# Performance work log

Measured on AMD Instinct MI355X. Metric: run time of the kernel, lower is better.

## Reference

```python
import jax, jax.numpy as jnp
import numpy as np
import math

D_MODEL = 128
N_HEADS = 8
D_K = D_MODEL // N_HEADS
D_FF = 512
N_LAYERS = 3
N_BUCKETS = 32
EPS = 1e-5
NEG_INF = -1e9
SCALE = 1.0 / math.sqrt(D_K)


def _hier_adj_np(N, L=8):
    # deterministic hierarchical edges from ExpanderGraphBuilder.build_hierarchical_edges
    stride = max(1, int(math.sqrt(N / L)))
    layer_size = N // L if L <= N else 1
    A = np.zeros((N, N), dtype=np.float32)
    for l in range(min(L, N)):
        start = l * layer_size
        end = min(start + layer_size, N)
        for i in range(start, end):
            A[i, max(start, i - stride):min(end, i + stride + 1)] = 1.0
            A[i, i] = 0.0
    return np.maximum(A, A.T)


def _build_mask(h, depot_idx=0):
    # h: (B,N,D). Returns additive mask (B,N+1,N+1) incl. global node.
    B, N, _ = h.shape
    k = min(max(1, math.ceil(math.log2(N))), N - 1)
    sq = jnp.sum(h * h, axis=-1)
    d2 = sq[:, :, None] + sq[:, None, :] - 2.0 * jnp.einsum('bnd,bmd->bnm', h, h)
    d2 = d2 + jnp.where(jnp.eye(N, dtype=bool), jnp.inf, 0.0)
    _, knn_idx = jax.lax.top_k(-d2, k)  # (B,N,k) nearest neighbors
    b_ix = jnp.arange(B)[:, None, None]
    i_ix = jnp.arange(N)[None, :, None]
    adj = jnp.zeros((B, N, N), dtype=h.dtype).at[b_ix, i_ix, knn_idx].set(1.0)
    adj = jnp.maximum(adj, adj.transpose(0, 2, 1))  # symmetrize knn
    adj = jnp.maximum(adj, jnp.asarray(_hier_adj_np(N))[None])
    adj = adj.at[:, depot_idx, :].set(1.0)
    adj = adj.at[:, :, depot_idx].set(1.0)
    adj = jnp.maximum(adj, jnp.eye(N, dtype=h.dtype)[None])
    full = jnp.ones((B, N + 1, N + 1), dtype=h.dtype).at[:, :N, :N].set(adj)
    return jnp.where(full > 0, 0.0, NEG_INF).astype(h.dtype)


def _inorm(x, w, b):
    # InstanceNorm1d over node dim per channel (x: (B,N1,D))
    mu = jnp.mean(x, axis=1, keepdims=True)
    var = jnp.mean(jnp.square(x - mu), axis=1, keepdims=True)
    return (x - mu) * jax.lax.rsqrt(var + EPS) * w + b


def _ega_layer(hg, bucket, mask, Wq, Wk, Wv, Wo, emb, W1, b1, W2, b2, n1w, n1b, n2w, n2b):
    B, N1, D = hg.shape
    heads = lambda x: x.reshape(B, N1, N_HEADS, D_K).transpose(0, 2, 1, 3)
    Q, K, V = heads(hg @ Wq.T), heads(hg @ Wk.T), heads(hg @ Wv.T)
    scores = jnp.einsum('bhnd,bhmd->bhnm', Q, K) * SCALE
    # rel_scores[b,h,i,j] = <Q[b,h,i], emb[bucket[b,i,j], h]> : contract with the
    # 32-entry table first, then gather - same math, no (B,H,N,N,Dk) intermediate.
    qe = jnp.einsum('bhnd,khd->bhnk', Q, emb.reshape(N_BUCKETS, N_HEADS, D_K))
    rel = jnp.take_along_axis(qe, jnp.broadcast_to(bucket[:, None], (B, N_HEADS, N1, N1)), axis=3)
    attn = jax.nn.softmax(scores + rel + mask[:, None], axis=-1)
    ctx = jnp.einsum('bhnm,bhmd->bhnd', attn, V).transpose(0, 2, 1, 3).reshape(B, N1, D)
    h1 = _inorm(hg + ctx @ Wo.T, n1w, n1b)
    ffn = jax.nn.relu(h1 @ W1.T + b1) @ W2.T + b2
    return _inorm(h1 + ffn, n2w, n2b)


def _forward(coords, in_W, in_b, gnode, Wq, Wk, Wv, Wo, emb, W1, b1, W2, b2,
             n1_w, n1_b, n2_w, n2_b, out_W, out_b):
    B, N, _ = coords.shape
    h = coords @ in_W.T + in_b
    g = jnp.broadcast_to(gnode, (B, 1, D_MODEL)).astype(h.dtype)
    # distance buckets over coords extended with the global node at (0,0)
    coords_ext = jnp.concatenate([coords, jnp.zeros((B, 1, 2), coords.dtype)], axis=1)
    diff = coords_ext[:, :, None, :] - coords_ext[:, None, :, :]
    dist = jax.lax.stop_gradient(jnp.sqrt(jnp.sum(diff * diff, axis=-1)))
    bucket = jnp.clip((dist * N_BUCKETS).astype(jnp.int32), 0, N_BUCKETS - 1)  # (B,N+1,N+1)
    pools = []
    for l in range(N_LAYERS):
        g = g + h.mean(axis=1, keepdims=True)
        hg = jnp.concatenate([h, g], axis=1)
        mask = _build_mask(jax.lax.stop_gradient(h))  # torch builds adj via .item(): detached
        hg = _ega_layer(hg, bucket, mask, Wq[l], Wk[l], Wv[l], Wo[l], emb[l],
                        W1[l], b1[l], W2[l], b2[l], n1_w[l], n1_b[l], n2_w[l], n2_b[l])
        h, g = hg[:, :N], hg[:, N:]
        pools.append(h.mean(axis=1))
    p_multi = jnp.stack(pools, axis=1).mean(axis=1)
    E_static = (h + p_multi[:, None, :]) @ out_W.T + out_b
    return E_static, p_multi


def setup_inputs():
    key = jax.random.key(0)
    ks = jax.random.split(key, 24)
    B, N, L = 2, 1024, N_LAYERS
    def nrm(k, shape, s=0.05):
        return jax.random.normal(k, shape, dtype=jnp.float32) * s
    return {
        'coords': jax.random.uniform(ks[0], (B, N, 2), dtype=jnp.float32),
        'in_W': nrm(ks[1], (D_MODEL, 2), 0.5),
        'in_b': nrm(ks[2], (D_MODEL,)),
        'gnode': nrm(ks[3], (1, 1, D_MODEL), 0.2),
        'Wq': nrm(ks[4], (L, D_MODEL, D_MODEL)),
        'Wk': nrm(ks[5], (L, D_MODEL, D_MODEL)),
        'Wv': nrm(ks[6], (L, D_MODEL, D_MODEL)),
        'Wo': nrm(ks[7], (L, D_MODEL, D_MODEL)),
        'emb': nrm(ks[8], (L, N_BUCKETS, N_HEADS * D_K)),
        'W1': nrm(ks[9], (L, D_FF, D_MODEL)),
        'b1': nrm(ks[10], (L, D_FF)),
        'W2': nrm(ks[11], (L, D_MODEL, D_FF)),
        'b2': nrm(ks[12], (L, D_MODEL)),
        'n1_w': jnp.ones((L, D_MODEL), jnp.float32) + nrm(ks[13], (L, D_MODEL)),
        'n1_b': nrm(ks[14], (L, D_MODEL)),
        'n2_w': jnp.ones((L, D_MODEL), jnp.float32) + nrm(ks[15], (L, D_MODEL)),
        'n2_b': nrm(ks[16], (L, D_MODEL)),
        'out_W': nrm(ks[17], (D_MODEL, D_MODEL)),
        'out_b': nrm(ks[18], (D_MODEL,)),
    }


def reference(coords, in_W, in_b, gnode, Wq, Wk, Wv, Wo, emb, W1, b1, W2, b2,
              n1_w, n1_b, n2_w, n2_b, out_W, out_b):
    return _forward(coords, in_W, in_b, gnode, Wq, Wk, Wv, Wo, emb, W1, b1, W2, b2,
                    n1_w, n1_b, n2_w, n2_b, out_W, out_b)
```

## Files before the change

kernel.cpp:

```cpp
#include <hip/hip_runtime.h>

#define BB 2
#define NN 1024
#define N1 1025
#define DM 128
#define NH 8
#define DK 16
#define DFF 512
#define NBUK 32
#define NLAYERS 3
#define KNN_K 10
#define ADJW 17
#define BSTR 1088
#define NSPLIT 8
#define BIGF 3.0e38f
#define SM_OFF 24.0f

#define PWQ_OFF 0
#define PWK_OFF 49152
#define PWV_OFF 98304
#define PWO_OFF 147456
#define PW1_OFF 196608
#define PW2_OFF 393216
#define PWOUT_OFF 589824
#define PWQE_OFF 606208
#define PW_TOT 704512

#define PBLK 344
#define NBNODE 1024
#define EBLK (NBNODE + BB)
#define BBLK 8713

#define KSEL_BLK 512
#define QKV_GX 33
#define QKV_BLK (QKV_GX * 40)
#define OSUM_N (BB * NH * N1 * 16)
#define ZTOT (OSUM_N + BB * NH * N1)

typedef __attribute__((ext_vector_type(8))) short bf8;
typedef __attribute__((ext_vector_type(4))) float f4;
typedef unsigned short u16;
typedef unsigned int u32;

__device__ __forceinline__ u16 f2bf(float x) {
  unsigned u = __float_as_uint(x);
  return (u16)((u + 0x7fff + ((u >> 16) & 1)) >> 16);
}
__device__ __forceinline__ float bf2f(u16 u) {
  return __uint_as_float(((unsigned)u) << 16);
}
__device__ __forceinline__ bf8 mk8(ushort4 a, ushort4 b) {
  bf8 r;
  r[0] = (short)a.x; r[1] = (short)a.y; r[2] = (short)a.z; r[3] = (short)a.w;
  r[4] = (short)b.x; r[5] = (short)b.y; r[6] = (short)b.z; r[7] = (short)b.w;
  return r;
}

__global__ __launch_bounds__(256) void init_kernel(
    const float* __restrict__ coords, const float* __restrict__ inW,
    const float* __restrict__ inb, const float* __restrict__ gnode,
    const float* __restrict__ Wq, const float* __restrict__ Wk,
    const float* __restrict__ Wv, const float* __restrict__ Wo,
    const float* __restrict__ W1, const float* __restrict__ W2,
    const float* __restrict__ oW, const float* __restrict__ emb,
    u16* __restrict__ PH, u16* __restrict__ PL,
    float* __restrict__ X, u16* __restrict__ XH, u16* __restrict__ XM,
    u16* __restrict__ XL, unsigned char* __restrict__ buckp) {
  int blk = blockIdx.x;
  if (blk < PBLK) {
    int idx = blk * 256 + threadIdx.x;
    if (idx >= 88064) return;
    if (idx >= 75776) {
      int rel = idx - 75776;
      int lane = rel & 63, g = rel >> 6;
      int ks = g & 3, nt = g >> 2;
      int n = nt * 16 + (lane & 15);
      int k = ks * 32 + (lane >> 4) * 8;
      int l = n >> 8; int c = n & 255; int h = c >> 5, bk = c & 31;
      const float* e = emb + ((size_t)l * NBUK + bk) * DM + h * DK;
      const float* wq = Wq + ((size_t)l * DM + h * DK) * DM;
      u16* ph = PH + (size_t)idx * 8;
      u16* pl = PL + (size_t)idx * 8;
      #pragma unroll
      for (int q = 0; q < 8; ++q) {
        float s = 0.f;
        #pragma unroll
        for (int d = 0; d < DK; ++d) s += e[d] * wq[(size_t)d * DM + k + q];
        u16 hh = f2bf(s);
        ph[q] = hh;
        pl[q] = f2bf(s - bf2f(hh));
      }
      return;
    }
    const float* W; int rel, Kdim;
    if (idx < 24576) {
      int seg = idx / 6144; rel = idx % 6144; Kdim = 128;
      W = seg == 0 ? Wq : seg == 1 ? Wk : seg == 2 ? Wv : Wo;
    } else if (idx < 49152) { rel = idx - 24576; Kdim = 128; W = W1; }
    else if (idx < 73728)   { rel = idx - 49152; Kdim = 512; W = W2; }
    else                    { rel = idx - 73728; Kdim = 128; W = oW; }
    int lane = rel & 63;
    int g = rel >> 6;
    int ksteps = Kdim >> 5;
    int ks = g % ksteps, nt = g / ksteps;
    int n = nt * 16 + (lane & 15);
    int k = ks * 32 + (lane >> 4) * 8;
    const float* p = W + (size_t)n * Kdim + k;
    u16* ph = PH + (size_t)idx * 8;
    u16* pl = PL + (size_t)idx * 8;
    #pragma unroll
    for (int q = 0; q < 8; ++q) {
      float x = p[q];
      u16 hh = f2bf(x);
      ph[q] = hh;
      pl[q] = f2bf(x - bf2f(hh));
    }
    return;
  }
  if (blk < PBLK + EBLK) {
    int eb = blk - PBLK;
    if (eb >= NBNODE) {
      int b = eb - NBNODE;
      int t = threadIdx.x;
      if (t >= 128) return;
      int lane = t & 63;
      float sx = 0.f, sy = 0.f;
      for (int n = lane; n < NN; n += 64) {
        float2 c = *(const float2*)(coords + (size_t)(b * NN + n) * 2);
        sx += c.x; sy += c.y;
      }
      #pragma unroll
      for (int o = 1; o < 64; o <<= 1) { sx += __shfl_xor(sx, o); sy += __shfl_xor(sy, o); }
      float mx = sx * (1.0f / NN), my = sy * (1.0f / NN);
      int d = t;
      size_t id = ((size_t)b * N1 + NN) * DM + d;
      float v = gnode[d] + inb[d] + mx * inW[d * 2 + 0] + my * inW[d * 2 + 1];
      X[id] = v;
      u16 hh = f2bf(v); float r1 = v - bf2f(hh);
      u16 mm = f2bf(r1);
      XH[id] = hh; XM[id] = mm; XL[id] = f2bf(r1 - bf2f(mm));
      return;
    }
    int idx = eb * 256 + threadIdx.x;
    if (idx >= BB * NN * DM) return;
    int d = idx % DM; int r = idx / DM; int n = r % NN; int b = r / NN;
    float cx = coords[(b * NN + n) * 2 + 0], cy = coords[(b * NN + n) * 2 + 1];
    size_t id = ((size_t)b * N1 + n) * DM + d;
    float v = cx * inW[d * 2 + 0] + cy * inW[d * 2 + 1] + inb[d];
    X[id] = v;
    u16 hh = f2bf(v); float r1 = v - bf2f(hh);
    u16 mm = f2bf(r1);
    XH[id] = hh; XM[id] = mm; XL[id] = f2bf(r1 - bf2f(mm));
    return;
  }
  int idx = (blk - PBLK - EBLK) * 256 + threadIdx.x;
  if (idx >= BB * N1 * BSTR) return;
  int j = idx % BSTR; int r = idx / BSTR; int i = r % N1; int b = r / N1;
  unsigned char v = 0;
  if (j < N1) {
    float xi = 0.f, yi = 0.f, xj = 0.f, yj = 0.f;
    if (i < NN) { xi = coords[(b * NN + i) * 2]; yi = coords[(b * NN + i) * 2 + 1]; }
    if (j < NN) { xj = coords[(b * NN + j) * 2]; yj = coords[(b * NN + j) * 2 + 1]; }
    float dx = xi - xj, dy = yi - yj;
    float dist = sqrtf(dx * dx + dy * dy);
    int bu = (int)(dist * 32.0f);
    bu = bu < 0 ? 0 : (bu > 31 ? 31 : bu);
    v = (unsigned char)bu;
  }
  buckp[idx] = v;
}

__global__ __launch_bounds__(256) void gram_kernel(
    const u16* __restrict__ XH, const u16* __restrict__ XM, const u16* __restrict__ XL,
    unsigned long long* __restrict__ adj, float* __restrict__ d2) {
  __shared__ __align__(16) u16 AsH[32][72];
  __shared__ __align__(16) u16 AsM[32][72];
  __shared__ __align__(16) u16 AsL[32][72];
  __shared__ __align__(16) u16 BsH[64][72];
  __shared__ __align__(16) u16 BsM[64][72];
  __shared__ __align__(16) u16 BsL[64][72];
  __shared__ float sqS[64];
  int b = blockIdx.z;
  int m0 = blockIdx.x * 32, n0 = blockIdx.y * 64;
  size_t boff = (size_t)b * N1;
  int t = threadIdx.x;

  {
    int flat = blockIdx.x + 32 * (blockIdx.y + 16 * blockIdx.z);
    int tid = flat * 256 + t;
    if (tid < BB * N1 * ADJW) adj[tid] = 0ull;
  }

  int lane = t & 63, w = t >> 6;
  int wm = (w >> 1) * 16, wn = (w & 1) * 32;
  int quad = lane >> 4, r16 = lane & 15;

  f4 acc0 = {0.f, 0.f, 0.f, 0.f}, acc1 = {0.f, 0.f, 0.f, 0.f};
  int ar = t >> 3, as_ = (t & 7) * 8;
  int br = t >> 2, bs_ = (t & 3) * 16;
  int sqrow = t >> 2, sqk = (t & 3) * 16;
  float mySq = 0.f;

  for (int k0 = 0; k0 < DM; k0 += 64) {
    {
      size_t src = (boff + m0 + ar) * DM + k0 + as_;
      *(bf8*)&AsH[ar][as_] = *(const bf8*)(XH + src);
      *(bf8*)&AsM[ar][as_] = *(const bf8*)(XM + src);
      *(bf8*)&AsL[ar][as_] = *(const bf8*)(XL + src);
    }
    {
      size_t src = (boff + n0 + br) * DM + k0 + bs_;
      *(bf8*)&BsH[br][bs_] = *(const bf8*)(XH + src);
      *(bf8*)&BsH[br][bs_ + 8] = *(const bf8*)(XH + src + 8);
      *(bf8*)&BsM[br][bs_] = *(const bf8*)(XM + src);
      *(bf8*)&BsM[br][bs_ + 8] = *(const bf8*)(XM + src + 8);
      *(bf8*)&BsL[br][bs_] = *(const bf8*)(XL + src);
      *(bf8*)&BsL[br][bs_ + 8] = *(const bf8*)(XL + src + 8);
    }
    __syncthreads();
    #pragma unroll
    for (int ks = 0; ks < 64; ks += 16) {
      int seg = (quad & 1) * 8;
      bf8 aHM = *(const bf8*)((quad < 2) ? &AsH[wm + r16][ks + seg] : &AsM[wm + r16][ks + seg]);
      bf8 aHL = *(const bf8*)((quad < 2) ? &AsH[wm + r16][ks + seg] : &AsL[wm + r16][ks + seg]);
      #pragma unroll
      for (int tt = 0; tt < 2; ++tt) {
        int nr = wn + tt * 16 + r16;
        bf8 bH = *(const bf8*)&BsH[nr][ks + seg];
        bf8 bM = *(const bf8*)&BsM[nr][ks + seg];
        bf8 b3 = *(const bf8*)((quad < 2) ? &BsL[nr][ks + seg] : &BsH[nr][ks + seg]);
        f4& a = tt ? acc1 : acc0;
        a = __builtin_amdgcn_mfma_f32_16x16x32_bf16(aHM, bH, a, 0, 0, 0);
        a = __builtin_amdgcn_mfma_f32_16x16x32_bf16(aHM, bM, a, 0, 0, 0);
        a = __builtin_amdgcn_mfma_f32_16x16x32_bf16(aHL, b3, a, 0, 0, 0);
      }
    }
    #pragma unroll
    for (int half = 0; half < 2; ++half) {
      bf8 hv = *(const bf8*)&BsH[sqrow][sqk + half * 8];
      bf8 mv = *(const bf8*)&BsM[sqrow][sqk + half * 8];
      bf8 lv = *(const bf8*)&BsL[sqrow][sqk + half * 8];
      #pragma unroll
      for (int q = 0; q < 8; ++q) {
        float x = (bf2f((u16)hv[q]) + bf2f((u16)mv[q])) + bf2f((u16)lv[q]);
        mySq += x * x;
      }
    }
    __syncthreads();
  }
  mySq += __shfl_xor(mySq, 1);
  mySq += __shfl_xor(mySq, 2);
  if ((t & 3) == 0) sqS[sqrow] = mySq;
  __syncthreads();

  #pragma unroll
  for (int tt = 0; tt < 2; ++tt) {
    f4 a = tt ? acc1 : acc0;
    int nl = wn + tt * 16 + r16;
    int n = n0 + nl;
    float sj = sqS[nl];
    #pragma unroll
    for (int reg = 0; reg < 4; ++reg) {
      int m = m0 + wm + quad * 4 + reg;
      float v = (m == n) ? BIGF : (sj - 2.f * a[reg]);
      d2[((size_t)b * NN + m) * NN + n] = v;
    }
  }
}

__global__ __launch_bounds__(256) void knnqkv_kernel(
    const float* __restrict__ d2, unsigned long long* __restrict__ adj,
    const u16* __restrict__ AH, const u16* __restrict__ AL,
    const u16* __restrict__ Pbase_H, const u16* __restrict__ Pbase_L,
    size_t offQ, size_t offK, size_t offV, size_t offE,
    u16* __restrict__ QH, u16* __restrict__ QL,
    u16* __restrict__ KH, u16* __restrict__ KL, u16* __restrict__ Vbf,
    float* __restrict__ qe_all, float* __restrict__ zbuf, int M) {
  __shared__ float dd[4][NN];
  {
    int ztid = blockIdx.x * 256 + threadIdx.x;
    if (ztid < ZTOT) zbuf[ztid] = 0.f;
  }
  int blk = blockIdx.x;
  if (blk < KSEL_BLK) {
    int b = blk / (NN / 4);
    int i0 = (blk % (NN / 4)) * 4;
    int t = threadIdx.x, lane = t & 63, w = t >> 6;

    const float4* src = (const float4*)(d2 + ((size_t)b * NN + i0) * NN);
    float4* dst = (float4*)&dd[0][0];
    #pragma unroll
    for (int x = 0; x < 4; ++x) dst[t + x * 256] = src[t + x * 256];
    __syncthreads();

    int i = i0 + w;
    for (int it = 0; it < KNN_K; ++it) {
      float bv = BIGF; int bi = 0x3fffffff;
      for (int j = lane; j < NN; j += 64) {
        float v = dd[w][j];
        if (v < bv) { bv = v; bi = j; }
      }
      #pragma unroll
      for (int o = 1; o < 64; o <<= 1) {
        float ov = __shfl_xor(bv, o); int oi = __shfl_xor(bi, o);
        if (ov < bv || (ov == bv && oi < bi)) { bv = ov; bi = oi; }
      }
      if (lane == 0) {
        dd[w][bi] = BIGF;
        atomicOr(&adj[((size_t)b * N1 + i) * ADJW + (bi >> 6)], 1ull << (bi & 63));
        atomicOr(&adj[((size_t)b * N1 + bi) * ADJW + (i >> 6)], 1ull << (i & 63));
      }
    }
    return;
  }
  int rel = blk - KSEL_BLK;
  int gx = rel % QKV_GX;
  int y = rel / QKV_GX;
  int z, nt;
  if (y < 8) { z = 0; nt = y; }
  else if (y < 16) { z = 1; nt = y - 8; }
  else if (y < 24) { z = 2; nt = y - 16; }
  else { z = 3; nt = y - 24; }
  size_t woff = z == 0 ? offQ : (z == 1 ? offK : (z == 2 ? offV : offE));
  const u16* PH = Pbase_H + woff;
  const u16* PL = Pbase_L + woff;
  int lane = threadIdx.x & 63;
  int quad = lane >> 4, r16 = lane & 15;
  int mt = gx * 4 + (threadIdx.x >> 6);
  f4 acc = {0.f, 0.f, 0.f, 0.f};
  int m0 = mt * 16;
  int mrow = m0 + r16; if (mrow >= M) mrow = M - 1;
  const u16* aph = AH + (size_t)mrow * DM + quad * 8;
  const u16* apl = AL + (size_t)mrow * DM + quad * 8;
  const u16* ph = PH + ((size_t)nt * 4 * 64 + lane) * 8;
  const u16* pl = PL + ((size_t)nt * 4 * 64 + lane) * 8;
  #pragma unroll
  for (int ks = 0; ks < 4; ++ks) {
    bf8 aH = *(const bf8*)(aph);
    bf8 aL = *(const bf8*)(apl);
    aph += 32; apl += 32;
    bf8 bH = *(const bf8*)(ph + (size_t)ks * 512);
    bf8 bL = *(const bf8*)(pl + (size_t)ks * 512);
    acc = __builtin_amdgcn_mfma_f32_16x16x32_bf16(aH, bH, acc, 0, 0, 0);
    acc = __builtin_amdgcn_mfma_f32_16x16x32_bf16(aH, bL, acc, 0, 0, 0);
    acc = __builtin_amdgcn_mfma_f32_16x16x32_bf16(aL, bH, acc, 0, 0, 0);
  }
  if (m0 >= M) return;
  int n = nt * 16 + r16;
  #pragma unroll
  for (int reg = 0; reg < 4; ++reg) {
    int m = m0 + quad * 4 + reg;
    if (m >= M) continue;
    float v = acc[reg];
    if (z == 3) {
      int b = m / N1, nr = m % N1;
      int h = n >> 5, bk = n & 31;
      qe_all[(((size_t)b * NH + h) * N1 + nr) * 32 + bk] = v;
      continue;
    }
    size_t oi = (size_t)m * DM + n;
    if (z == 0) {
      float sv = v * 0.25f;
      u16 hh = f2bf(sv);
      QH[oi] = hh;
      QL[oi] = f2bf(sv - bf2f(hh));
    } else if (z == 1) {
      u16 hh = f2bf(v);
      KH[oi] = hh;
      KL[oi] = f2bf(v - bf2f(hh));
    } else {
      Vbf[oi] = f2bf(v);
    }
  }
}

__device__ __forceinline__ void gemm_dev16(
    const u16* __restrict__ AH, const u16* __restrict__ AL,
    const u16* __restrict__ PH, const u16* __restrict__ PL,
    const float* __restrict__ bias, const float* __restrict__ res,
    float* __restrict__ outF, u16* __restrict__ outH, u16* __restrict__ outL,
    int M, int Kdim, int Nout, int relu, int mt, int nt) {
  int lane = threadIdx.x & 63;
  int quad = lane >> 4, r16 = lane & 15;
  int ksteps = Kdim >> 5;
  f4 acc = {0.f, 0.f, 0.f, 0.f};

  int m0 = mt * 16;
  int mrow = m0 + r16; if (mrow >= M) mrow = M - 1;
  const u16* aph = AH + (size_t)mrow * Kdim + quad * 8;
  const u16* apl = AL + (size_t)mrow * Kdim + quad * 8;
  const u16* ph = PH + ((size_t)nt * ksteps * 64 + lane) * 8;
  const u16* pl = PL + ((size_t)nt * ksteps * 64 + lane) * 8;

  #pragma unroll 4
  for (int ks = 0; ks < ksteps; ++ks) {
    bf8 aH = *(const bf8*)(aph);
    bf8 aL = *(const bf8*)(apl);
    aph += 32; apl += 32;
    bf8 bH = *(const bf8*)(ph + (size_t)ks * 512);
    bf8 bL = *(const bf8*)(pl + (size_t)ks * 512);
    acc = __builtin_amdgcn_mfma_f32_16x16x32_bf16(aH, bH, acc, 0, 0, 0);
    acc = __builtin_amdgcn_mfma_f32_16x16x32_bf16(aH, bL, acc, 0, 0, 0);
    acc = __builtin_amdgcn_mfma_f32_16x16x32_bf16(aL, bH, acc, 0, 0, 0);
  }

  if (m0 >= M) return;
  int n = nt * 16 + r16;
  #pragma unroll
  for (int reg = 0; reg < 4; ++reg) {
    int m = m0 + quad * 4 + reg;
    if (m < M) {
      float v = acc[reg];
      if (bias) v += bias[n];
      if (relu) v = fmaxf(v, 0.f);
      if (res) v += res[(size_t)m * Nout + n];
      size_t oi = (size_t)m * Nout + n;
      if (outF) outF[oi] = v;
      if (outH) {
        u16 hh = f2bf(v);
        outH[oi] = hh;
        outL[oi] = f2bf(v - bf2f(hh));
      }
    }
  }
}

__global__ __launch_bounds__(256) void gemm_kernel(
    const u16* __restrict__ AH, const u16* __restrict__ AL,
    const u16* __restrict__ PH, const u16* __restrict__ PL,
    const float* __restrict__ bias, const float* __restrict__ res,
    float* __restrict__ outF, u16* __restrict__ outH, u16* __restrict__ outL,
    int M, int Kdim, int Nout, int relu) {
  gemm_dev16(AH, AL, PH, PL, bias, res, outF, outH, outL, M, Kdim, Nout, relu,
             blockIdx.x * 4 + (threadIdx.x >> 6), blockIdx.y);
}

__global__ __launch_bounds__(256) void gemm_wo_kernel(
    const float* __restrict__ Osum, const float* __restrict__ lsum,
    const u16* __restrict__ PH, const u16* __restrict__ PL,
    const float* __restrict__ res, float* __restrict__ outF, int M) {
  int lane = threadIdx.x & 63;
  int quad = lane >> 4, r16 = lane & 15;
  int mt = blockIdx.x * 4 + (threadIdx.x >> 6), nt = blockIdx.y;
  f4 acc = {0.f, 0.f, 0.f, 0.f};
  int m0 = mt * 16;
  int mrow = m0 + r16; if (mrow >= M) mrow = M - 1;
  int b = mrow / N1, nr = mrow % N1;
  const u16* ph = PH + ((size_t)nt * 4 * 64 + lane) * 8;
  const u16* pl = PL + ((size_t)nt * 4 * 64 + lane) * 8;
  #pragma unroll
  for (int ks = 0; ks < 4; ++ks) {
    int k = ks * 32 + quad * 8;
    int h = k >> 4, d0 = k & 15;
    size_t base = (size_t)(b * NH + h) * N1 + nr;
    float inv = 1.0f / lsum[base];
    const float* op = Osum + base * 16 + d0;
    bf8 aH, aL;
    #pragma unroll
    for (int j = 0; j < 8; ++j) {
      float v = op[j] * inv;
      u16 hh = f2bf(v);
      aH[j] = (short)hh;
      aL[j] = (short)f2bf(v - bf2f(hh));
    }
    bf8 bH = *(const bf8*)(ph + (size_t)ks * 512);
    bf8 bL = *(const bf8*)(pl + (size_t)ks * 512);
    acc = __builtin_amdgcn_mfma_f32_16x16x32_bf16(aH, bH, acc, 0, 0, 0);
    acc = __builtin_amdgcn_mfma_f32_16x16x32_bf16(aH, bL, acc, 0, 0, 0);
    acc = __builtin_amdgcn_mfma_f32_16x16x32_bf16(aL, bH, acc, 0, 0, 0);
  }
  if (m0 >= M) return;
  int n = nt * 16 + r16;
  #pragma unroll
  for (int reg = 0; reg < 4; ++reg) {
    int m = m0 + quad * 4 + reg;
    if (m < M) outF[(size_t)m * DM + n] = acc[reg] + res[(size_t)m * DM + n];
  }
}

#define CH 64
#define NCH 17
__global__ __launch_bounds__(128) void attn_kernel(
    const u16* __restrict__ QH, const u16* __restrict__ QL,
    const u16* __restrict__ KH, const u16* __restrict__ KL,
    const u16* __restrict__ Vbf, const float* __restrict__ qe_all,
    const unsigned char* __restrict__ buckp, const unsigned long long* __restrict__ adj,
    float* __restrict__ Osum, float* __restrict__ lsum) {
  __shared__ __align__(16) u16 KsHi[2][CH][20];
  __shared__ __align__(16) u16 KsLo[2][CH][20];
  __shared__ __align__(16) u16 Vt[2][DK][68];
  __shared__ __align__(16) u16 Ps[2][16][72];
  __shared__ __align__(16) float qe_s[2][16][36];
  __shared__ u32 maskS[32][6];
  __shared__ unsigned char buckS[2][32][68];

  int qt = blockIdx.x;
  int h = blockIdx.y & 7, b = blockIdx.y >> 3;
  int s = blockIdx.z;
  int c0 = (NCH * s) / NSPLIT, c1 = (NCH * (s + 1)) / NSPLIT;
  int nwm = 2 * (c1 - c0);
  int t = threadIdx.x, lane = t & 63, w = t >> 6;
  int quad = lane >> 4, r16 = lane & 15;
  int i0 = qt * 32;
  int iw = i0 + w * 16;
  int bh = b * NH + h;

  for (int x = t; x < 32 * nwm; x += 128) {
    int rr = x / nwm, ww = x % nwm;
    int gi = i0 + rr; if (gi > NN) gi = NN;
    int W = 2 * c0 + ww;
    u32 v;
    if (gi == 0 || gi == NN) {
      v = 0xffffffffu;
    } else {
      const u32* a32 = (const u32*)(adj + ((size_t)b * N1 + gi) * ADJW);
      v = a32[W];
      int bs = gi & ~127;
      int lo = gi - 11 < bs ? bs : gi - 11;
      int be = bs + 127;
      int hi = gi + 11 > be ? be : gi + 11;
      int aa = lo - 32 * W, bnd = hi - 32 * W;
      if (aa < 0) aa = 0; if (bnd > 31) bnd = 31;
      if (aa <= bnd) v |= (0xffffffffu << aa) & (0xffffffffu >> (31 - bnd));
      if (W == 0) v |= 1u;
      if (W == 32) v |= 1u;
      int dg = gi - 32 * W;
      if (dg >= 0 && dg < 32) v |= 1u << dg;
    }
    if (W == 32) v &= 1u;
    else if (W == 33) v = 0u;
    maskS[rr][ww] = v;
  }
  #pragma unroll
  for (int e = 0; e < 2; ++e) {
    int x = lane + e * 64;
    int rr = x >> 3, bk = (x & 7) * 4;
    int gi = iw + rr; if (gi > NN) gi = NN;
    f4 v = *(const f4*)(qe_all + (((size_t)b * NH + h) * N1 + gi) * 32 + bk);
    *(f4*)&qe_s[w][rr][bk] = v;
  }
  bf8 qfrag;
  {
    int gi = iw + r16; if (gi > NN) gi = NN;
    const u16* qsrc = (quad < 2 ? QH : QL) + ((size_t)(b * N1 + gi) * DM + h * DK + (quad & 1) * 8);
    qfrag = *(const bf8*)qsrc;
  }

  ushort4 khr[2], klr[2], vvr[2]; u32 bkr[4];
  auto load_chunk = [&](int c) {
    int j0 = c * CH;
    #pragma unroll
    for (int ii = 0; ii < 2; ++ii) {
      int x = t + ii * 128;
      int key = x >> 2, ds = (x & 3) * 4;
      int jg = j0 + key; if (jg > NN) jg = NN;
      size_t src = (size_t)(b * N1 + jg) * DM + h * DK + ds;
      khr[ii] = *(const ushort4*)(KH + src);
      klr[ii] = *(const ushort4*)(KL + src);
      vvr[ii] = *(const ushort4*)(Vbf + src);
    }
    #pragma unroll
    for (int ii = 0; ii < 4; ++ii) {
      int x = t + ii * 128;
      int rr = x >> 4, c4 = (x & 15) * 4;
      int gi = i0 + rr; if (gi > NN) gi = NN;
      bkr[ii] = *(const u32*)(buckp + ((size_t)b * N1 + gi) * BSTR + j0 + c4);
    }
  };
  auto store_chunk = [&](int pb) {
    #pragma unroll
    for (int ii = 0; ii < 2; ++ii) {
      int x = t + ii * 128;
      int key = x >> 2, ds = (x & 3) * 4;
      *(ushort4*)&KsHi[pb][key][ds] = khr[ii];
      *(ushort4*)&KsLo[pb][key][ds] = klr[ii];
      Vt[pb][ds + 0][key] = vvr[ii].x;
      Vt[pb][ds + 1][key] = vvr[ii].y;
      Vt[pb][ds + 2][key] = vvr[ii].z;
      Vt[pb][ds + 3][key] = vvr[ii].w;
    }
    #pragma unroll
    for (int ii = 0; ii < 4; ++ii) {
      int x = t + ii * 128;
      int rr = x >> 4, c4 = (x & 15) * 4;
      *(u32*)&buckS[pb][rr][c4] = bkr[ii];
    }
  };

  f4 Oacc = {0.f, 0.f, 0.f, 0.f};
  float lrun[4] = {0.f, 0.f, 0.f, 0.f};

  load_chunk(c0);
  store_chunk(0);

  for (int c = c0; c < c1; ++c) {
    int pb = (c - c0) & 1;
    bool pf = (c + 1 < c1);
    if (pf) load_chunk(c + 1);
    __syncthreads();

    f4 S[4];
    #pragma unroll
    for (int tt = 0; tt < 4; ++tt) {
      int key = tt * 16 + r16;
      int off = (quad & 1) * 8;
      bf8 bhv = mk8(*(const ushort4*)&KsHi[pb][key][off], *(const ushort4*)&KsHi[pb][key][off + 4]);
      bf8 blv = mk8(*(const ushort4*)&KsLo[pb][key][off], *(const ushort4*)&KsLo[pb][key][off + 4]);
      f4 z = {0.f, 0.f, 0.f, 0.f};
      z = __builtin_amdgcn_mfma_f32_16x16x32_bf16(qfrag, bhv, z, 0, 0, 0);
      z = __builtin_amdgcn_mfma_f32_16x16x32_bf16(qfrag, blv, z, 0, 0, 0);
      S[tt] = z;
    }

    #pragma unroll
    for (int rg = 0; rg < 4; ++rg) {
      int rowb = w * 16 + quad * 4 + rg;
      u32 mw0 = maskS[rowb][2 * (c - c0)];
      u32 mw1 = maskS[rowb][2 * (c - c0) + 1];
      float ps = 0.f;
      #pragma unroll
      for (int tt = 0; tt < 4; ++tt) {
        u32 mword = (tt & 2) ? mw1 : mw0;
        int bit = (tt & 1) * 16 + r16;
        int bk = buckS[pb][rowb][tt * 16 + r16] & 31;
        float rel = qe_s[w][quad * 4 + rg][bk];
        float sc = S[tt][rg] + rel;
        sc += ((mword >> bit) & 1u) ? 0.f : -1.0e9f;
        float p = __expf(sc - SM_OFF);
        ps += p;
        Ps[w][quad * 4 + rg][tt * 16 + r16] = f2bf(p);
      }
      #pragma unroll
      for (int o = 1; o < 16; o <<= 1) ps += __shfl_xor(ps, o);
      lrun[rg] += ps;
    }
    #pragma unroll
    for (int half = 0; half < 2; ++half) {
      bf8 pa = *(const bf8*)&Ps[w][r16][half * 32 + quad * 8];
      bf8 vb = mk8(*(const ushort4*)&Vt[pb][r16][half * 32 + quad * 8],
                   *(const ushort4*)&Vt[pb][r16][half * 32 + quad * 8 + 4]);
      Oacc = __builtin_amdgcn_mfma_f32_16x16x32_bf16(pa, vb, Oacc, 0, 0, 0);
    }

    if (pf) store_chunk(pb ^ 1);
  }

  #pragma unroll
  for (int rg = 0; rg < 4; ++rg) {
    int gi = i0 + w * 16 + quad * 4 + rg;
    if (gi < N1) {
      size_t base = (size_t)bh * N1 + gi;
      atomicAdd(&Osum[base * 16 + r16], Oacc[rg]);
      if (r16 == 0) atomicAdd(&lsum[base], lrun[rg]);
    }
  }
}

__global__ void inorm_kernel(float* __restrict__ X, const float* __restrict__ w,
                             const float* __restrict__ b_, float* __restrict__ pool,
                             int do_g, u16* __restrict__ oH, u16* __restrict__ oM,
                             u16* __restrict__ oL) {
  int d = blockIdx.x; int bb = blockIdx.y; int lane = threadIdx.x;
  float g_old = X[((size_t)bb * N1 + NN) * DM + d];
  float s = 0.f;
  for (int n = lane; n < N1; n += 64) s += X[((size_t)bb * N1 + n) * DM + d];
  #pragma unroll
  for (int o = 1; o < 64; o <<= 1) s += __shfl_xor(s, o);
  float mu = s * (1.0f / N1);
  float v = 0.f;
  for (int n = lane; n < N1; n += 64) {
    float tt = X[((size_t)bb * N1 + n) * DM + d] - mu;
    v += tt * tt;
  }
  #pragma unroll
  for (int o = 1; o < 64; o <<= 1) v += __shfl_xor(v, o);
  float var = v * (1.0f / N1);
  float scv = rsqrtf(var + 1e-5f) * w[d];
  float sh = b_[d];
  for (int n = lane; n < N1; n += 64) {
    size_t id = ((size_t)bb * N1 + n) * DM + d;
    float nv = (X[id] - mu) * scv + sh;
    X[id] = nv;
    if (oH) {
      u16 hh = f2bf(nv); float r1 = nv - bf2f(hh);
      u16 mm = f2bf(r1);
      oH[id] = hh;
      oM[id] = mm;
      if (oL) oL[id] = f2bf(r1 - bf2f(mm));
    }
  }
  if (lane == 0) {
    float hmean = ((s - g_old) * (1.0f / NN) - mu) * scv + sh;
    if (pool) pool[bb * DM + d] = hmean;
    if (do_g) X[((size_t)bb * N1 + NN) * DM + d] += hmean;
  }
}

__global__ __launch_bounds__(256) void gemm_final_kernel(
    const float* __restrict__ X, const float* __restrict__ pools,
    const u16* __restrict__ PH, const u16* __restrict__ PL,
    const float* __restrict__ bias, float* __restrict__ out, float* __restrict__ out_pm) {
  int t = threadIdx.x;
  if (blockIdx.x == 0 && blockIdx.y == 0) {
    float pmv = (pools[t] + pools[BB * DM + t] + pools[2 * BB * DM + t]) * (1.0f / 3.0f);
    out_pm[t] = pmv;
  }
  int lane = t & 63;
  int quad = lane >> 4, r16 = lane & 15;
  int mt = blockIdx.x * 4 + (t >> 6), nt = blockIdx.y;
  const int M = BB * NN;
  f4 acc = {0.f, 0.f, 0.f, 0.f};
  int m0 = mt * 16;
  int mrow = m0 + r16; if (mrow >= M) mrow = M - 1;
  int mb = mrow / NN, mn = mrow % NN;
  const float* xp = X + ((size_t)mb * N1 + mn) * DM + quad * 8;
  const float* pp = pools + mb * DM + quad * 8;
  const u16* ph = PH + ((size_t)nt * 4 * 64 + lane) * 8;
  const u16* pl = PL + ((size_t)nt * 4 * 64 + lane) * 8;
  #pragma unroll
  for (int ks = 0; ks < 4; ++ks) {
    bf8 aH, aL;
    #pragma unroll
    for (int half = 0; half < 2; ++half) {
      float4 xv = *(const float4*)(xp + ks * 32 + half * 4);
      float4 p0 = *(const float4*)(pp + ks * 32 + half * 4);
      float4 p1 = *(const float4*)(pp + BB * DM + ks * 32 + half * 4);
      float4 p2 = *(const float4*)(pp + 2 * BB * DM + ks * 32 + half * 4);
      float av[4] = {xv.x + (p0.x + p1.x + p2.x) * (1.0f / 3.0f),
                     xv.y + (p0.y + p1.y + p2.y) * (1.0f / 3.0f),
                     xv.z + (p0.z + p1.z + p2.z) * (1.0f / 3.0f),
                     xv.w + (p0.w + p1.w + p2.w) * (1.0f / 3.0f)};
      #pragma unroll
      for (int q = 0; q < 4; ++q) {
        u16 hh = f2bf(av[q]);
        aH[half * 4 + q] = (short)hh;
        aL[half * 4 + q] = (short)f2bf(av[q] - bf2f(hh));
      }
    }
    bf8 bH = *(const bf8*)(ph + (size_t)ks * 512);
    bf8 bL = *(const bf8*)(pl + (size_t)ks * 512);
    acc = __builtin_amdgcn_mfma_f32_16x16x32_bf16(aH, bH, acc, 0, 0, 0);
    acc = __builtin_amdgcn_mfma_f32_16x16x32_bf16(aH, bL, acc, 0, 0, 0);
    acc = __builtin_amdgcn_mfma_f32_16x16x32_bf16(aL, bH, acc, 0, 0, 0);
  }
  int n = nt * 16 + r16;
  #pragma unroll
  for (int reg = 0; reg < 4; ++reg) {
    int m = m0 + quad * 4 + reg;
    if (m < M) out[(size_t)m * DM + n] = acc[reg] + bias[n];
  }
}

extern "C" void kernel_launch(void* const* d_in, const int* in_sizes, int n_in,
                              void* d_out, int out_size, void* d_ws, size_t ws_size,
                              hipStream_t stream) {
  const float* coords = (const float*)d_in[0];
  const float* inW    = (const float*)d_in[1];
  const float* inb    = (const float*)d_in[2];
  const float* gnode  = (const float*)d_in[3];
  const float* Wq     = (const float*)d_in[4];
  const float* Wk     = (const float*)d_in[5];
  const float* Wv     = (const float*)d_in[6];
  const float* Wo     = (const float*)d_in[7];
  const float* emb    = (const float*)d_in[8];
  const float* W1     = (const float*)d_in[9];
  const float* b1     = (const float*)d_in[10];
  const float* W2     = (const float*)d_in[11];
  const float* b2     = (const float*)d_in[12];
  const float* n1w    = (const float*)d_in[13];
  const float* n1b    = (const float*)d_in[14];
  const float* n2w    = (const float*)d_in[15];
  const float* n2b    = (const float*)d_in[16];
  const float* outW   = (const float*)d_in[17];
  const float* outb   = (const float*)d_in[18];
  float* out = (float*)d_out;

  char* wsp = (char*)d_ws;
  size_t off = 0;
  auto alloc = [&](size_t bytes) -> void* {
    off = (off + 255) & ~(size_t)255;
    void* p = wsp + off;
    off += bytes;
    return p;
  };
  const size_t XB = (size_t)BB * N1 * DM * 4;
  const size_t HB = (size_t)BB * N1 * DM * 2;
  float* X0   = (float*)alloc(XB);
  float* X1   = (float*)alloc(XB);
  float* Yb   = (float*)alloc(XB);
  u16* XH = (u16*)alloc(HB); u16* XM = (u16*)alloc(HB); u16* XL = (u16*)alloc(HB);
  u16* QH = (u16*)alloc(HB); u16* QL = (u16*)alloc(HB);
  u16* KH = (u16*)alloc(HB); u16* KL = (u16*)alloc(HB);
  u16* Vbf = (u16*)alloc(HB);
  u16* YbH = (u16*)alloc(HB); u16* YbL = (u16*)alloc(HB);
  u16* FbH = (u16*)alloc((size_t)BB * N1 * DFF * 2);
  u16* FbL = (u16*)alloc((size_t)BB * N1 * DFF * 2);
  unsigned char* buckp = (unsigned char*)alloc((size_t)BB * N1 * BSTR);
  unsigned long long* adj = (unsigned long long*)alloc((size_t)BB * N1 * ADJW * 8);
  float* pools = (float*)alloc((size_t)NLAYERS * BB * DM * 4);
  float* qe_all = (float*)alloc((size_t)BB * NH * N1 * 32 * 4);
  float* zbuf = (float*)alloc((size_t)ZTOT * 4);
  u16* PH = (u16*)alloc((size_t)PW_TOT * 2);
  u16* PL = (u16*)alloc((size_t)PW_TOT * 2);
  float* d2 = (float*)alloc((size_t)BB * NN * NN * 4);

  float* Osum = zbuf;
  float* lsum = zbuf + OSUM_N;

  init_kernel<<<PBLK + EBLK + BBLK, 256, 0, stream>>>(
      coords, inW, inb, gnode, Wq, Wk, Wv, Wo, W1, W2, outW, emb,
      PH, PL, X0, XH, XM, XL, buckp);

  float* Xin = X0; float* Xout = X1;
  const int M = BB * N1;
  const int GX = 33;
  for (int l = 0; l < NLAYERS; ++l) {
    gram_kernel<<<dim3(32, 16, BB), 256, 0, stream>>>(XH, XM, XL, adj, d2);

    knnqkv_kernel<<<KSEL_BLK + QKV_BLK, 256, 0, stream>>>(
        d2, adj, XH, XM, PH, PL,
        (size_t)PWQ_OFF + (size_t)l * DM * DM,
        (size_t)PWK_OFF + (size_t)l * DM * DM,
        (size_t)PWV_OFF + (size_t)l * DM * DM,
        (size_t)PWQE_OFF + (size_t)l * 256 * DM,
        QH, QL, KH, KL, Vbf, qe_all, zbuf, M);

    attn_kernel<<<dim3(33, NH * BB, NSPLIT), 128, 0, stream>>>(
        QH, QL, KH, KL, Vbf, qe_all, buckp, adj, Osum, lsum);

    gemm_wo_kernel<<<dim3(GX, 8), 256, 0, stream>>>(
        Osum, lsum, PH + PWO_OFF + (size_t)l * DM * DM, PL + PWO_OFF + (size_t)l * DM * DM,
        Xin, Yb, M);
    inorm_kernel<<<dim3(DM, BB), 64, 0, stream>>>(Yb, n1w + l * DM, n1b + l * DM,
                                                  nullptr, 0, YbH, YbL, nullptr);

    gemm_kernel<<<dim3(GX, 32), 256, 0, stream>>>(
        YbH, YbL, PH + PW1_OFF + (size_t)l * DFF * DM, PL + PW1_OFF + (size_t)l * DFF * DM,
        b1 + l * DFF, nullptr, nullptr, FbH, FbL, M, DM, DFF, 1);
    gemm_kernel<<<dim3(GX, 8), 256, 0, stream>>>(
        FbH, FbL, PH + PW2_OFF + (size_t)l * DM * DFF, PL + PW2_OFF + (size_t)l * DM * DFF,
        b2 + l * DM, Yb, Xout, nullptr, nullptr, M, DFF, DM, 0);
    inorm_kernel<<<dim3(DM, BB), 64, 0, stream>>>(Xout, n2w + l * DM, n2b + l * DM,
                                                  pools + (size_t)l * BB * DM, 1,
                                                  XH, XM, XL);

    float* t2 = Xin; Xin = Xout; Xout = t2;
  }

  gemm_final_kernel<<<dim3(32, 8), 256, 0, stream>>>(
      Xin, pools, PH + PWOUT_OFF, PL + PWOUT_OFF, outb, out, out + (size_t)BB * NN * DM);
}
```

Measured before the change: 467.6 us.

## Fuse first instance norm into Wo epilogue stats and W1/W2 prologues

Removes the standalone instance-norm launch after the attention output projection. The Wo GEMM now accumulates per-channel sum and sum-of-squares with shared and global atomics. The W1 and W2 GEMMs recompute mean and rstd from these sums and apply the normalization on the fly, W1 to its inputs and W2 to its residual. This saves one kernel launch per layer and the bf16 hi/lo Yb round trip. In exchange it uses a one-pass E[x^2]-mu^2 variance that is less numerically stable, and it relies on the stats buffer being zeroed every layer (it sits inside zbuf, which is presumably cleared by knnqkv).

```diff
diff --git a/kernel.cpp b/kernel.cpp
--- a/kernel.cpp
+++ b/kernel.cpp
@@ -35,7 +35,9 @@
 #define QKV_GX 33
 #define QKV_BLK (QKV_GX * 40)
 #define OSUM_N (BB * NH * N1 * 16)
-#define ZTOT (OSUM_N + BB * NH * N1)
+#define LSUM_N (BB * NH * N1)
+#define STAT_N (BB * DM)
+#define ZTOT (OSUM_N + LSUM_N + 2 * STAT_N)
 
 typedef __attribute__((ext_vector_type(8))) short bf8;
 typedef __attribute__((ext_vector_type(4))) float f4;
@@ -374,26 +376,166 @@
   }
 }
 
-__device__ __forceinline__ void gemm_dev16(
+__global__ __launch_bounds__(256) void gemm_wo_kernel(
+    const float* __restrict__ Osum, const float* __restrict__ lsum,
+    const u16* __restrict__ PH, const u16* __restrict__ PL,
+    const float* __restrict__ res, float* __restrict__ outF,
+    float* __restrict__ sumY, float* __restrict__ sumY2, int M) {
+  __shared__ float sA[2][16], sQ[2][16];
+  int t = threadIdx.x;
+  if (t < 32) {
+    sA[t >> 4][t & 15] = 0.f;
+    sQ[t >> 4][t & 15] = 0.f;
+  }
+  __syncthreads();
+  int lane = t & 63;
+  int quad = lane >> 4, r16 = lane & 15;
+  int mt = blockIdx.x * 4 + (t >> 6), nt = blockIdx.y;
+  f4 acc = {0.f, 0.f, 0.f, 0.f};
+  int m0 = mt * 16;
+  int mrow = m0 + r16; if (mrow >= M) mrow = M - 1;
+  int b = mrow / N1, nr = mrow % N1;
+  const u16* ph = PH + ((size_t)nt * 4 * 64 + lane) * 8;
+  const u16* pl = PL + ((size_t)nt * 4 * 64 + lane) * 8;
+  #pragma unroll
+  for (int ks = 0; ks < 4; ++ks) {
+    int k = ks * 32 + quad * 8;
+    int h = k >> 4, d0 = k & 15;
+    size_t base = (size_t)(b * NH + h) * N1 + nr;
+    float inv = 1.0f / lsum[base];
+    const float* op = Osum + base * 16 + d0;
+    bf8 aH, aL;
+    #pragma unroll
+    for (int j = 0; j < 8; ++j) {
+      float v = op[j] * inv;
+      u16 hh = f2bf(v);
+      aH[j] = (short)hh;
+      aL[j] = (short)f2bf(v - bf2f(hh));
+    }
+    bf8 bH = *(const bf8*)(ph + (size_t)ks * 512);
+    bf8 bL = *(const bf8*)(pl + (size_t)ks * 512);
+    acc = __builtin_amdgcn_mfma_f32_16x16x32_bf16(aH, bH, acc, 0, 0, 0);
+    acc = __builtin_amdgcn_mfma_f32_16x16x32_bf16(aH, bL, acc, 0, 0, 0);
+    acc = __builtin_amdgcn_mfma_f32_16x16x32_bf16(aL, bH, acc, 0, 0, 0);
+  }
+  int n = nt * 16 + r16;
+  if (m0 < M) {
+    #pragma unroll
+    for (int reg = 0; reg < 4; ++reg) {
+      int m = m0 + quad * 4 + reg;
+      if (m < M) {
+        float v = acc[reg] + res[(size_t)m * DM + n];
+        outF[(size_t)m * DM + n] = v;
+        int mb2 = m / N1;
+        atomicAdd(&sA[mb2][r16], v);
+        atomicAdd(&sQ[mb2][r16], v * v);
+      }
+    }
+  }
+  __syncthreads();
+  if (t < 32) {
+    int bb = t >> 4, d = nt * 16 + (t & 15);
+    atomicAdd(&sumY[bb * DM + d], sA[bb][t & 15]);
+    atomicAdd(&sumY2[bb * DM + d], sQ[bb][t & 15]);
+  }
+}
+
+__global__ __launch_bounds__(256) void gemm_w1_kernel(
+    const float* __restrict__ Yb, const float* __restrict__ sumY,
+    const float* __restrict__ sumY2, const float* __restrict__ n1w,
+    const float* __restrict__ n1b,
+    const u16* __restrict__ PH, const u16* __restrict__ PL,
+    const float* __restrict__ bias,
+    u16* __restrict__ outH, u16* __restrict__ outL, int M) {
+  __shared__ float muS[STAT_N], scvS[STAT_N], shS[STAT_N];
+  int t = threadIdx.x;
+  {
+    float mu = sumY[t] * (1.0f / N1);
+    float var = sumY2[t] * (1.0f / N1) - mu * mu;
+    int d = t & (DM - 1);
+    muS[t] = mu;
+    scvS[t] = rsqrtf(var + 1e-5f) * n1w[d];
+    shS[t] = n1b[d];
+  }
+  __syncthreads();
+  int lane = t & 63;
+  int quad = lane >> 4, r16 = lane & 15;
+  int mt = blockIdx.x * 4 + (t >> 6), nt = blockIdx.y;
+  f4 acc = {0.f, 0.f, 0.f, 0.f};
+  int m0 = mt * 16;
+  int mrow = m0 + r16; if (mrow >= M) mrow = M - 1;
+  int b = mrow / N1;
+  const float* yp = Yb + (size_t)mrow * DM + quad * 8;
+  const u16* ph = PH + ((size_t)nt * 4 * 64 + lane) * 8;
+  const u16* pl = PL + ((size_t)nt * 4 * 64 + lane) * 8;
+  #pragma unroll
+  for (int ks = 0; ks < 4; ++ks) {
+    int k = ks * 32 + quad * 8;
+    bf8 aH, aL;
+    #pragma unroll
+    for (int half = 0; half < 2; ++half) {
+      float4 yv = *(const float4*)(yp + ks * 32 + half * 4);
+      float ya[4] = {yv.x, yv.y, yv.z, yv.w};
+      #pragma unroll
+      for (int q = 0; q < 4; ++q) {
+        int sidx = b * DM + k + half * 4 + q;
+        float nv = (ya[q] - muS[sidx]) * scvS[sidx] + shS[sidx];
+        u16 hh = f2bf(nv);
+        aH[half * 4 + q] = (short)hh;
+        aL[half * 4 + q] = (short)f2bf(nv - bf2f(hh));
+      }
+    }
+    bf8 bH = *(const bf8*)(ph + (size_t)ks * 512);
+    bf8 bL = *(const bf8*)(pl + (size_t)ks * 512);
+    acc = __builtin_amdgcn_mfma_f32_16x16x32_bf16(aH, bH, acc, 0, 0, 0);
+    acc = __builtin_amdgcn_mfma_f32_16x16x32_bf16(aH, bL, acc, 0, 0, 0);
+    acc = __builtin_amdgcn_mfma_f32_16x16x32_bf16(aL, bH, acc, 0, 0, 0);
+  }
+  if (m0 >= M) return;
+  int n = nt * 16 + r16;
+  #pragma unroll
+  for (int reg = 0; reg < 4; ++reg) {
+    int m = m0 + quad * 4 + reg;
+    if (m < M) {
+      float v = fmaxf(acc[reg] + bias[n], 0.f);
+      size_t oi = (size_t)m * DFF + n;
+      u16 hh = f2bf(v);
+      outH[oi] = hh;
+      outL[oi] = f2bf(v - bf2f(hh));
+    }
+  }
+}
+
+__global__ __launch_bounds__(256) void gemm_w2_kernel(
     const u16* __restrict__ AH, const u16* __restrict__ AL,
     const u16* __restrict__ PH, const u16* __restrict__ PL,
-    const float* __restrict__ bias, const float* __restrict__ res,
-    float* __restrict__ outF, u16* __restrict__ outH, u16* __restrict__ outL,
-    int M, int Kdim, int Nout, int relu, int mt, int nt) {
-  int lane = threadIdx.x & 63;
+    const float* __restrict__ bias, const float* __restrict__ Yb,
+    const float* __restrict__ sumY, const float* __restrict__ sumY2,
+    const float* __restrict__ n1w, const float* __restrict__ n1b,
+    float* __restrict__ outF, int M) {
+  __shared__ float muS[STAT_N], scvS[STAT_N], shS[STAT_N];
+  int t = threadIdx.x;
+  {
+    float mu = sumY[t] * (1.0f / N1);
+    float var = sumY2[t] * (1.0f / N1) - mu * mu;
+    int d = t & (DM - 1);
+    muS[t] = mu;
+    scvS[t] = rsqrtf(var + 1e-5f) * n1w[d];
+    shS[t] = n1b[d];
+  }
+  __syncthreads();
+  int lane = t & 63;
   int quad = lane >> 4, r16 = lane & 15;
-  int ksteps = Kdim >> 5;
+  int mt = blockIdx.x * 4 + (t >> 6), nt = blockIdx.y;
   f4 acc = {0.f, 0.f, 0.f, 0.f};
-
   int m0 = mt * 16;
   int mrow = m0 + r16; if (mrow >= M) mrow = M - 1;
-  const u16* aph = AH + (size_t)mrow * Kdim + quad * 8;
-  const u16* apl = AL + (size_t)mrow * Kdim + quad * 8;
-  const u16* ph = PH + ((size_t)nt * ksteps * 64 + lane) * 8;
-  const u16* pl = PL + ((size_t)nt * ksteps * 64 + lane) * 8;
-
+  const u16* aph = AH + (size_t)mrow * DFF + quad * 8;
+  const u16* apl = AL + (size_t)mrow * DFF + quad * 8;
+  const u16* ph = PH + ((size_t)nt * 16 * 64 + lane) * 8;
+  const u16* pl = PL + ((size_t)nt * 16 * 64 + lane) * 8;
   #pragma unroll 4
-  for (int ks = 0; ks < ksteps; ++ks) {
+  for (int ks = 0; ks < 16; ++ks) {
     bf8 aH = *(const bf8*)(aph);
     bf8 aL = *(const bf8*)(apl);
     aph += 32; apl += 32;
@@ -403,78 +545,17 @@
     acc = __builtin_amdgcn_mfma_f32_16x16x32_bf16(aH, bL, acc, 0, 0, 0);
     acc = __builtin_amdgcn_mfma_f32_16x16x32_bf16(aL, bH, acc, 0, 0, 0);
   }
-
   if (m0 >= M) return;
   int n = nt * 16 + r16;
   #pragma unroll
   for (int reg = 0; reg < 4; ++reg) {
     int m = m0 + quad * 4 + reg;
     if (m < M) {
-      float v = acc[reg];
-      if (bias) v += bias[n];
-      if (relu) v = fmaxf(v, 0.f);
-      if (res) v += res[(size_t)m * Nout + n];
-      size_t oi = (size_t)m * Nout + n;
-      if (outF) outF[oi] = v;
-      if (outH) {
-        u16 hh = f2bf(v);
-        outH[oi] = hh;
-        outL[oi] = f2bf(v - bf2f(hh));
-      }
-    }
-  }
-}
-
-__global__ __launch_bounds__(256) void gemm_kernel(
-    const u16* __restrict__ AH, const u16* __restrict__ AL,
-    const u16* __restrict__ PH, const u16* __restrict__ PL,
-    const float* __restrict__ bias, const float* __restrict__ res,
-    float* __restrict__ outF, u16* __restrict__ outH, u16* __restrict__ outL,
-    int M, int Kdim, int Nout, int relu) {
-  gemm_dev16(AH, AL, PH, PL, bias, res, outF, outH, outL, M, Kdim, Nout, relu,
-             blockIdx.x * 4 + (threadIdx.x >> 6), blockIdx.y);
-}
-
-__global__ __launch_bounds__(256) void gemm_wo_kernel(
-    const float* __restrict__ Osum, const float* __restrict__ lsum,
-    const u16* __restrict__ PH, const u16* __restrict__ PL,
-    const float* __restrict__ res, float* __restrict__ outF, int M) {
-  int lane = threadIdx.x & 63;
-  int quad = lane >> 4, r16 = lane & 15;
-  int mt = blockIdx.x * 4 + (threadIdx.x >> 6), nt = blockIdx.y;
-  f4 acc = {0.f, 0.f, 0.f, 0.f};
-  int m0 = mt * 16;
-  int mrow = m0 + r16; if (mrow >= M) mrow = M - 1;
-  int b = mrow / N1, nr = mrow % N1;
-  const u16* ph = PH + ((size_t)nt * 4 * 64 + lane) * 8;
-  const u16* pl = PL + ((size_t)nt * 4 * 64 + lane) * 8;
-  #pragma unroll
-  for (int ks = 0; ks < 4; ++ks) {
-    int k = ks * 32 + quad * 8;
-    int h = k >> 4, d0 = k & 15;
-    size_t base = (size_t)(b * NH + h) * N1 + nr;
-    float inv = 1.0f / lsum[base];
-    const float* op = Osum + base * 16 + d0;
-    bf8 aH, aL;
-    #pragma unroll
-    for (int j = 0; j < 8; ++j) {
-      float v = op[j] * inv;
-      u16 hh = f2bf(v);
-      aH[j] = (short)hh;
-      aL[j] = (short)f2bf(v - bf2f(hh));
-    }
-    bf8 bH = *(const bf8*)(ph + (size_t)ks * 512);
-    bf8 bL = *(const bf8*)(pl + (size_t)ks * 512);
-    acc = __builtin_amdgcn_mfma_f32_16x16x32_bf16(aH, bH, acc, 0, 0, 0);
-    acc = __builtin_amdgcn_mfma_f32_16x16x32_bf16(aH, bL, acc, 0, 0, 0);
-    acc = __builtin_amdgcn_mfma_f32_16x16x32_bf16(aL, bH, acc, 0, 0, 0);
-  }
-  if (m0 >= M) return;
-  int n = nt * 16 + r16;
-  #pragma unroll
-  for (int reg = 0; reg < 4; ++reg) {
-    int m = m0 + quad * 4 + reg;
-    if (m < M) outF[(size_t)m * DM + n] = acc[reg] + res[(size_t)m * DM + n];
+      int b = m / N1;
+      int sidx = b * DM + n;
+      float h1 = (Yb[(size_t)m * DM + n] - muS[sidx]) * scvS[sidx] + shS[sidx];
+      outF[(size_t)m * DM + n] = acc[reg] + bias[n] + h1;
+    }
   }
 }
 
@@ -792,7 +873,6 @@
   u16* QH = (u16*)alloc(HB); u16* QL = (u16*)alloc(HB);
   u16* KH = (u16*)alloc(HB); u16* KL = (u16*)alloc(HB);
   u16* Vbf = (u16*)alloc(HB);
-  u16* YbH = (u16*)alloc(HB); u16* YbL = (u16*)alloc(HB);
   u16* FbH = (u16*)alloc((size_t)BB * N1 * DFF * 2);
   u16* FbL = (u16*)alloc((size_t)BB * N1 * DFF * 2);
   unsigned char* buckp = (unsigned char*)alloc((size_t)BB * N1 * BSTR);
@@ -806,6 +886,8 @@
 
   float* Osum = zbuf;
   float* lsum = zbuf + OSUM_N;
+  float* sumY = zbuf + OSUM_N + LSUM_N;
+  float* sumY2 = sumY + STAT_N;
 
   init_kernel<<<PBLK + EBLK + BBLK, 256, 0, stream>>>(
       coords, inW, inb, gnode, Wq, Wk, Wv, Wo, W1, W2, outW, emb,
@@ -830,16 +912,17 @@
 
     gemm_wo_kernel<<<dim3(GX, 8), 256, 0, stream>>>(
         Osum, lsum, PH + PWO_OFF + (size_t)l * DM * DM, PL + PWO_OFF + (size_t)l * DM * DM,
-        Xin, Yb, M);
-    inorm_kernel<<<dim3(DM, BB), 64, 0, stream>>>(Yb, n1w + l * DM, n1b + l * DM,
-                                                  nullptr, 0, YbH, YbL, nullptr);
-
-    gemm_kernel<<<dim3(GX, 32), 256, 0, stream>>>(
-        YbH, YbL, PH + PW1_OFF + (size_t)l * DFF * DM, PL + PW1_OFF + (size_t)l * DFF * DM,
-        b1 + l * DFF, nullptr, nullptr, FbH, FbL, M, DM, DFF, 1);
-    gemm_kernel<<<dim3(GX, 8), 256, 0, stream>>>(
+        Xin, Yb, sumY, sumY2, M);
+
+    gemm_w1_kernel<<<dim3(GX, 32), 256, 0, stream>>>(
+        Yb, sumY, sumY2, n1w + l * DM, n1b + l * DM,
+        PH + PW1_OFF + (size_t)l * DFF * DM, PL + PW1_OFF + (size_t)l * DFF * DM,
+        b1 + l * DFF, FbH, FbL, M);
+
+    gemm_w2_kernel<<<dim3(GX, 8), 256, 0, stream>>>(
         FbH, FbL, PH + PW2_OFF + (size_t)l * DM * DFF, PL + PW2_OFF + (size_t)l * DM * DFF,
-        b2 + l * DM, Yb, Xout, nullptr, nullptr, M, DFF, DM, 0);
+        b2 + l * DM, Yb, sumY, sumY2, n1w + l * DM, n1b + l * DM, Xout, M);
+
     inorm_kernel<<<dim3(DM, BB), 64, 0, stream>>>(Xout, n2w + l * DM, n2b + l * DM,
                                                   pools + (size_t)l * BB * DM, 1,
                                                   XH, XM, XL);
```

Result: faster. 422.3 us (-9.7%).
